# Kernel tuning notes

Hardware: AMD Instinct MI355X
Metric: run time of the kernel (lower is better)

Reference implementation:

```python
import jax, jax.numpy as jnp
import numpy as np

N = 768
C = 256  # in_features == out_features (required by Linear(in_features+3, 1))

def _leaky(x):
    return jnp.where(x >= 0, x, 0.2 * x)

def setup_inputs() -> dict:
    key = jax.random.key(0)
    ks = jax.random.split(key, 10)
    features = jax.random.normal(ks[0], (N, C), dtype=jnp.float32)
    coordinates = jax.random.normal(ks[1], (N, 3), dtype=jnp.float32)
    adj = jax.random.uniform(ks[2], (N, N), dtype=jnp.float32)  # unused by forward, kept for signature fidelity
    # Learned params
    FC = jax.random.normal(ks[3], (C, C), dtype=jnp.float32) * (1.414 / jnp.sqrt(C))
    # Conv1d(2,1,kernel=1): weight [out=1, in=2, k=1] -> 2 scalars + bias
    fc_w = jax.random.normal(ks[4], (2,), dtype=jnp.float32) * 0.5
    fc_b = jax.random.normal(ks[5], (1,), dtype=jnp.float32) * 0.1
    sc_w = jax.random.normal(ks[6], (2,), dtype=jnp.float32) * 0.5
    sc_b = jax.random.normal(ks[7], (1,), dtype=jnp.float32) * 0.1
    # Linear(C+3, 1)
    lin_w = jax.random.normal(ks[8], (C + 3,), dtype=jnp.float32) * (1.0 / jnp.sqrt(C + 3))
    lin_b = jax.random.normal(ks[9], (1,), dtype=jnp.float32) * 0.1
    return {"features": features, "coordinates": coordinates, "adj": adj,
            "FC": FC, "fc_w": fc_w, "fc_b": fc_b, "sc_w": sc_w, "sc_b": sc_b,
            "lin_w": lin_w, "lin_b": lin_b}

def reference(features, coordinates, adj, FC, fc_w, fc_b, sc_w, sc_b, lin_w, lin_b):
    n = features.shape[0]
    f_input = features @ FC  # [N, C]
    # torch's repeat(1,N).view + repeat(N,1) builds pairs (i, j); the 1x1 Conv1d over
    # the 2 stacked channels is exactly w0*x_i + w1*x_j + b, then LeakyReLU(0.2).
    f_map = _leaky(fc_w[0] * f_input[:, None, :] + fc_w[1] * f_input[None, :, :] + fc_b[0])  # [N,N,C]
    s_map = _leaky(sc_w[0] * coordinates[:, None, :] + sc_w[1] * coordinates[None, :, :] + sc_b[0])  # [N,N,3]
    # Linear(C+3, 1) on cat([f_map, s_map], -1), then LeakyReLU -> [N, N]
    scores = _leaky(jnp.einsum('ijc,c->ij', f_map, lin_w[:f_input.shape[1]])
                    + jnp.einsum('ijk,k->ij', s_map, lin_w[f_input.shape[1]:])
                    + lin_b[0])
    attention = jax.nn.softmax(scores, axis=1)  # row softmax (dim=1)
    h_prime = attention @ f_input  # [N, C]
    return jax.nn.elu(h_prime)  # concat=True path
```

## Files before the change

kernel.cpp:

```cpp
#include <hip/hip_runtime.h>
#include <math.h>

#define NN 768
#define CC 256
#define TI 3
#define RT 12
#define JCC 256
#define NJC 3
#define PSTR 20

__device__ __forceinline__ float leaky(float x) { return x >= 0.0f ? x : 0.2f * x; }

__device__ __forceinline__ float waveMax(float v) {
    #pragma unroll
    for (int o = 32; o > 0; o >>= 1) v = fmaxf(v, __shfl_xor(v, o, 64));
    return v;
}
__device__ __forceinline__ float waveSum(float v) {
    #pragma unroll
    for (int o = 32; o > 0; o >>= 1) v += __shfl_xor(v, o, 64);
    return v;
}

__device__ __forceinline__ void acc_row(float4& a, float ur, float w4, const float4& gv) {
    a.x = fmaf(w4, fabsf(ur + gv.x), a.x);
    a.y = fmaf(w4, fabsf(ur + gv.y), a.y);
    a.z = fmaf(w4, fabsf(ur + gv.z), a.z);
    a.w = fmaf(w4, fabsf(ur + gv.w), a.w);
}
__device__ __forceinline__ void fma4(float4& h, float e, const float4& fv) {
    h.x = fmaf(e, fv.x, h.x);
    h.y = fmaf(e, fv.y, h.y);
    h.z = fmaf(e, fv.z, h.z);
    h.w = fmaf(e, fv.w, h.w);
}

__global__ __launch_bounds__(768) void k_prep(
    const float* __restrict__ features,
    const float* __restrict__ FC,
    const float* __restrict__ fc_w,
    const float* __restrict__ fc_b,
    const float* __restrict__ lin_w,
    float* __restrict__ f,
    float* __restrict__ g,
    float* __restrict__ D0,
    float* __restrict__ D1,
    float4* __restrict__ ut4)
{
    __shared__ float sA[TI * CC];
    __shared__ float sF[TI * CC];
    __shared__ float sredD[12], sredW[12];

    const int t  = threadIdx.x;
    const int r  = t >> 8;
    const int c  = t & 255;
    const int i0 = blockIdx.x * TI;

    sA[r * CC + c] = features[(i0 + r) * CC + c];
    __syncthreads();

    float a = 0.f;
    const float* fcp = FC + c;
    const float* ap  = sA + r * CC;
    #pragma unroll 8
    for (int k = 0; k < CC; ++k)
        a = fmaf(ap[k], fcp[k * CC], a);

    const float w1 = fc_w[1], b = fc_b[0];
    f[(i0 + r) * CC + c] = a;
    g[c * NN + i0 + r]   = fmaf(w1, a, b);
    sF[r * CC + c] = a;

    const float lw = lin_w[c];
    float dv = waveSum(lw * a);
    float wv = waveSum(lw);
    const int wid = t >> 6;
    if ((t & 63) == 0) { sredD[wid] = dv; sredW[wid] = wv; }
    __syncthreads();
    if (t < TI) {
        float D = sredD[t*4] + sredD[t*4+1] + sredD[t*4+2] + sredD[t*4+3];
        float W = sredW[t*4] + sredW[t*4+1] + sredW[t*4+2] + sredW[t*4+3];
        D0[i0 + t] = fc_w[0] * D;
        D1[i0 + t] = fmaf(w1, D, b * W);
    }
    if (t < CC) {
        const float w0 = fc_w[0];
        ut4[blockIdx.x * CC + t] = make_float4(w0 * sF[t],
                                               w0 * sF[CC + t],
                                               w0 * sF[2*CC + t],
                                               0.4f * lin_w[t]);
    }
}

__global__ __launch_bounds__(256) void k_attn(
    const float* __restrict__ f,
    const float* __restrict__ g,
    const float4* __restrict__ ut4,
    const float* __restrict__ D0,
    const float* __restrict__ D1,
    const float* __restrict__ coords,
    const float* __restrict__ sc_w,
    const float* __restrict__ sc_b,
    const float* __restrict__ lin_w,
    const float* __restrict__ lin_b,
    float* __restrict__ hp,
    float* __restrict__ Mp,
    float* __restrict__ Lp)
{
    __shared__ float4 su4[4][CC];
    __shared__ float  sred[4][RT][CC];
    __shared__ float  pe[JCC][PSTR];
    __shared__ float  sredm[4][RT];
    __shared__ float  sreds[4][RT];

    const int t    = threadIdx.x;
    const int it   = blockIdx.x & 63;
    const int jc   = blockIdx.x >> 6;
    const int i0   = it * RT;
    const int jb   = jc * JCC;
    const int w    = t >> 6;
    const int lane = t & 63;

    #pragma unroll
    for (int q = 0; q < 4; ++q)
        su4[q][t] = ut4[(size_t)(it * 4 + q) * CC + t];
    __syncthreads();

    float4 acc[RT];
    #pragma unroll
    for (int r = 0; r < RT; ++r) acc[r] = make_float4(0.f, 0.f, 0.f, 0.f);
    const float4* gq = (const float4*)g + (size_t)(w << 6) * (NN/4) + (jb >> 2) + lane;
    #pragma unroll 4
    for (int cc = 0; cc < 64; ++cc) {
        float4 gv = gq[(size_t)cc * (NN/4)];
        const int c = (w << 6) + cc;
        #pragma unroll
        for (int q = 0; q < 4; ++q) {
            float4 u = su4[q][c];
            acc_row(acc[3*q+0], u.x, u.w, gv);
            acc_row(acc[3*q+1], u.y, u.w, gv);
            acc_row(acc[3*q+2], u.z, u.w, gv);
        }
    }
    #pragma unroll
    for (int r = 0; r < RT; ++r)
        *(float4*)&sred[w][r][4*lane] = acc[r];
    __syncthreads();

    const int j = jb + t;
    const float sw0 = sc_w[0], sw1 = sc_w[1], sb = sc_b[0], lb = lin_b[0];
    const float lw30 = lin_w[CC], lw31 = lin_w[CC+1], lw32 = lin_w[CC+2];
    const float cj0 = fmaf(sw1, coords[j*3+0], sb);
    const float cj1 = fmaf(sw1, coords[j*3+1], sb);
    const float cj2 = fmaf(sw1, coords[j*3+2], sb);
    const float d1  = D1[j];
    float scv[RT];
    #pragma unroll
    for (int r = 0; r < RT; ++r) {
        const int i = i0 + r;
        float a = sred[0][r][t] + sred[1][r][t] + sred[2][r][t] + sred[3][r][t];
        float sd = lw30 * leaky(fmaf(sw0, coords[i*3+0], cj0))
                 + lw31 * leaky(fmaf(sw0, coords[i*3+1], cj1))
                 + lw32 * leaky(fmaf(sw0, coords[i*3+2], cj2));
        scv[r] = leaky(a + sd + 0.6f * (D0[i] + d1) + lb);
    }

    #pragma unroll
    for (int r = 0; r < RT; ++r) {
        float v = waveMax(scv[r]);
        if (lane == 0) sredm[w][r] = v;
    }
    __syncthreads();
    float m[RT];
    #pragma unroll
    for (int r = 0; r < RT; ++r)
        m[r] = fmaxf(fmaxf(sredm[0][r], sredm[1][r]),
                     fmaxf(sredm[2][r], sredm[3][r]));
    float e[RT];
    #pragma unroll
    for (int r = 0; r < RT; ++r) {
        e[r] = __expf(scv[r] - m[r]);
        pe[t][r] = e[r];
    }
    #pragma unroll
    for (int r = 0; r < RT; ++r) {
        float v = waveSum(e[r]);
        if (lane == 0) sreds[w][r] = v;
    }
    __syncthreads();
    if (t < RT) {
        float l  = sreds[0][t] + sreds[1][t] + sreds[2][t] + sreds[3][t];
        float mm = fmaxf(fmaxf(sredm[0][t], sredm[1][t]),
                         fmaxf(sredm[2][t], sredm[3][t]));
        Mp[(i0 + t) * NJC + jc] = mm;
        Lp[(i0 + t) * NJC + jc] = l;
    }

    float4 h[RT];
    #pragma unroll
    for (int r = 0; r < RT; ++r) h[r] = make_float4(0.f, 0.f, 0.f, 0.f);
    const float4* f4 = (const float4*)f;
    const int jsl = w * 64;
    #pragma unroll 2
    for (int jx = 0; jx < 64; ++jx) {
        const int jl = jsl + jx;
        float4 fv = f4[(size_t)(jb + jl) * 64 + lane];
        const float4* pe4 = (const float4*)&pe[jl][0];
        float4 e0 = pe4[0], e1 = pe4[1], e2 = pe4[2];
        fma4(h[0],  e0.x, fv); fma4(h[1],  e0.y, fv);
        fma4(h[2],  e0.z, fv); fma4(h[3],  e0.w, fv);
        fma4(h[4],  e1.x, fv); fma4(h[5],  e1.y, fv);
        fma4(h[6],  e1.z, fv); fma4(h[7],  e1.w, fv);
        fma4(h[8],  e2.x, fv); fma4(h[9],  e2.y, fv);
        fma4(h[10], e2.z, fv); fma4(h[11], e2.w, fv);
    }
    #pragma unroll
    for (int r = 0; r < RT; ++r)
        *(float4*)&sred[w][r][4*lane] = h[r];
    __syncthreads();

    #pragma unroll
    for (int r = 0; r < RT; ++r) {
        float hh = sred[0][r][t] + sred[1][r][t] + sred[2][r][t] + sred[3][r][t];
        hp[((size_t)jc * NN + i0 + r) * CC + t] = hh;
    }
}

__global__ __launch_bounds__(256) void k_comb(
    const float* __restrict__ hp,
    const float* __restrict__ Mp,
    const float* __restrict__ Lp,
    float* __restrict__ out)
{
    const int t = threadIdx.x;
    const int i = blockIdx.x;

    float m0 = Mp[i*NJC+0], m1 = Mp[i*NJC+1], m2 = Mp[i*NJC+2];
    float M  = fmaxf(fmaxf(m0, m1), m2);
    float w0 = __expf(m0 - M), w1 = __expf(m1 - M), w2 = __expf(m2 - M);
    float den = w0*Lp[i*NJC+0] + w1*Lp[i*NJC+1] + w2*Lp[i*NJC+2];
    float inv = 1.0f / den;

    float num = w0 * hp[((size_t)0*NN + i)*CC + t]
              + w1 * hp[((size_t)1*NN + i)*CC + t]
              + w2 * hp[((size_t)2*NN + i)*CC + t];
    float v = num * inv;
    out[i*CC + t] = (v > 0.f) ? v : (__expf(v) - 1.0f);
}

extern "C" void kernel_launch(void* const* d_in, const int* in_sizes, int n_in,
                              void* d_out, int out_size, void* d_ws, size_t ws_size,
                              hipStream_t stream) {
    const float* features = (const float*)d_in[0];
    const float* coords   = (const float*)d_in[1];
    const float* FC       = (const float*)d_in[3];
    const float* fc_w     = (const float*)d_in[4];
    const float* fc_b     = (const float*)d_in[5];
    const float* sc_w     = (const float*)d_in[6];
    const float* sc_b     = (const float*)d_in[7];
    const float* lin_w    = (const float*)d_in[8];
    const float* lin_b    = (const float*)d_in[9];
    float* out = (float*)d_out;

    float* f  = (float*)d_ws;
    float* g  = f  + NN*CC;
    float* D0 = g  + CC*NN;
    float* D1 = D0 + NN;
    float* Mp = D1 + NN;
    float* Lp = Mp + NN*NJC;
    float* hp = Lp + NN*NJC;
    float4* ut4;
    {
        size_t off = (size_t)((char*)(hp + (size_t)NJC*NN*CC) - (char*)d_ws);
        off = (off + 15) & ~(size_t)15;
        ut4 = (float4*)((char*)d_ws + off);
    }

    k_prep<<<NN/TI, 768, 0, stream>>>(features, FC, fc_w, fc_b, lin_w, f, g, D0, D1, ut4);
    k_attn<<<(NN/RT)*NJC, 256, 0, stream>>>(f, g, ut4, D0, D1, coords, sc_w, sc_b,
                                            lin_w, lin_b, hp, Mp, Lp);
    k_comb<<<NN, 256, 0, stream>>>(hp, Mp, Lp, out);
}
```

Measured before the change: 128.8 us.

## Halve attention row and column tiles and broadcast u via readlane

```diff
diff --git a/kernel.cpp b/kernel.cpp
--- a/kernel.cpp
+++ b/kernel.cpp
@@ -4,12 +4,15 @@
 #define NN 768
 #define CC 256
 #define TI 3
-#define RT 12
-#define JCC 256
-#define NJC 3
-#define PSTR 20
+#define RT 6
+#define JC 128
+#define NJC 6
 
 __device__ __forceinline__ float leaky(float x) { return x >= 0.0f ? x : 0.2f * x; }
+
+__device__ __forceinline__ float rl(float v, int l) {
+    return __uint_as_float(__builtin_amdgcn_readlane(__float_as_uint(v), l));
+}
 
 __device__ __forceinline__ float waveMax(float v) {
     #pragma unroll
@@ -22,12 +25,6 @@
     return v;
 }
 
-__device__ __forceinline__ void acc_row(float4& a, float ur, float w4, const float4& gv) {
-    a.x = fmaf(w4, fabsf(ur + gv.x), a.x);
-    a.y = fmaf(w4, fabsf(ur + gv.y), a.y);
-    a.z = fmaf(w4, fabsf(ur + gv.z), a.z);
-    a.w = fmaf(w4, fabsf(ur + gv.w), a.w);
-}
 __device__ __forceinline__ void fma4(float4& h, float e, const float4& fv) {
     h.x = fmaf(e, fv.x, h.x);
     h.y = fmaf(e, fv.y, h.y);
@@ -107,121 +104,133 @@
     float* __restrict__ Mp,
     float* __restrict__ Lp)
 {
-    __shared__ float4 su4[4][CC];
-    __shared__ float  sred[4][RT][CC];
-    __shared__ float  pe[JCC][PSTR];
-    __shared__ float  sredm[4][RT];
-    __shared__ float  sreds[4][RT];
+    __shared__ float spart[4][RT][JC];
+    __shared__ float hpart[4][RT][CC];
+    __shared__ float pe[JC][8];
+    __shared__ float sredm[4][3];
+    __shared__ float sreds[4][3];
 
     const int t    = threadIdx.x;
-    const int it   = blockIdx.x & 63;
-    const int jc   = blockIdx.x >> 6;
+    const int it   = blockIdx.x & 127;
+    const int jc   = blockIdx.x >> 7;
     const int i0   = it * RT;
-    const int jb   = jc * JCC;
+    const int jb   = jc * JC;
     const int w    = t >> 6;
     const int lane = t & 63;
 
-    #pragma unroll
-    for (int q = 0; q < 4; ++q)
-        su4[q][t] = ut4[(size_t)(it * 4 + q) * CC + t];
-    __syncthreads();
-
-    float4 acc[RT];
-    #pragma unroll
-    for (int r = 0; r < RT; ++r) acc[r] = make_float4(0.f, 0.f, 0.f, 0.f);
-    const float4* gq = (const float4*)g + (size_t)(w << 6) * (NN/4) + (jb >> 2) + lane;
-    #pragma unroll 4
+    float4 ur0 = ut4[(size_t)(it*2 + 0) * CC + (w << 6) + lane];
+    float4 ur1 = ut4[(size_t)(it*2 + 1) * CC + (w << 6) + lane];
+
+    float2 acc[RT];
+    #pragma unroll
+    for (int r = 0; r < RT; ++r) acc[r] = make_float2(0.f, 0.f);
+    const float2* gq = (const float2*)g + (size_t)(w << 6) * (NN/2) + (jb >> 1) + lane;
+    #pragma unroll 8
     for (int cc = 0; cc < 64; ++cc) {
-        float4 gv = gq[(size_t)cc * (NN/4)];
-        const int c = (w << 6) + cc;
-        #pragma unroll
-        for (int q = 0; q < 4; ++q) {
-            float4 u = su4[q][c];
-            acc_row(acc[3*q+0], u.x, u.w, gv);
-            acc_row(acc[3*q+1], u.y, u.w, gv);
-            acc_row(acc[3*q+2], u.z, u.w, gv);
-        }
-    }
-    #pragma unroll
-    for (int r = 0; r < RT; ++r)
-        *(float4*)&sred[w][r][4*lane] = acc[r];
-    __syncthreads();
-
-    const int j = jb + t;
+        float2 gv = gq[cc * (NN/2)];
+        float w4 = rl(ur0.w, cc);
+        float u0 = rl(ur0.x, cc), u1 = rl(ur0.y, cc), u2 = rl(ur0.z, cc);
+        float u3 = rl(ur1.x, cc), u4 = rl(ur1.y, cc), u5 = rl(ur1.z, cc);
+        acc[0].x = fmaf(w4, fabsf(u0 + gv.x), acc[0].x);
+        acc[0].y = fmaf(w4, fabsf(u0 + gv.y), acc[0].y);
+        acc[1].x = fmaf(w4, fabsf(u1 + gv.x), acc[1].x);
+        acc[1].y = fmaf(w4, fabsf(u1 + gv.y), acc[1].y);
+        acc[2].x = fmaf(w4, fabsf(u2 + gv.x), acc[2].x);
+        acc[2].y = fmaf(w4, fabsf(u2 + gv.y), acc[2].y);
+        acc[3].x = fmaf(w4, fabsf(u3 + gv.x), acc[3].x);
+        acc[3].y = fmaf(w4, fabsf(u3 + gv.y), acc[3].y);
+        acc[4].x = fmaf(w4, fabsf(u4 + gv.x), acc[4].x);
+        acc[4].y = fmaf(w4, fabsf(u4 + gv.y), acc[4].y);
+        acc[5].x = fmaf(w4, fabsf(u5 + gv.x), acc[5].x);
+        acc[5].y = fmaf(w4, fabsf(u5 + gv.y), acc[5].y);
+    }
+    #pragma unroll
+    for (int r = 0; r < RT; ++r) {
+        spart[w][r][2*lane+0] = acc[r].x;
+        spart[w][r][2*lane+1] = acc[r].y;
+    }
+    __syncthreads();
+
+    const int jl   = t & 127;
+    const int half = t >> 7;
+    const int rb   = 3 * half;
+    const int j    = jb + jl;
+    float accs[3];
+    #pragma unroll
+    for (int rr = 0; rr < 3; ++rr)
+        accs[rr] = spart[0][rb+rr][jl] + spart[1][rb+rr][jl]
+                 + spart[2][rb+rr][jl] + spart[3][rb+rr][jl];
+
     const float sw0 = sc_w[0], sw1 = sc_w[1], sb = sc_b[0], lb = lin_b[0];
     const float lw30 = lin_w[CC], lw31 = lin_w[CC+1], lw32 = lin_w[CC+2];
     const float cj0 = fmaf(sw1, coords[j*3+0], sb);
     const float cj1 = fmaf(sw1, coords[j*3+1], sb);
     const float cj2 = fmaf(sw1, coords[j*3+2], sb);
     const float d1  = D1[j];
-    float scv[RT];
-    #pragma unroll
-    for (int r = 0; r < RT; ++r) {
-        const int i = i0 + r;
-        float a = sred[0][r][t] + sred[1][r][t] + sred[2][r][t] + sred[3][r][t];
+    float scv[3];
+    #pragma unroll
+    for (int rr = 0; rr < 3; ++rr) {
+        const int i = i0 + rb + rr;
         float sd = lw30 * leaky(fmaf(sw0, coords[i*3+0], cj0))
                  + lw31 * leaky(fmaf(sw0, coords[i*3+1], cj1))
                  + lw32 * leaky(fmaf(sw0, coords[i*3+2], cj2));
-        scv[r] = leaky(a + sd + 0.6f * (D0[i] + d1) + lb);
-    }
-
-    #pragma unroll
-    for (int r = 0; r < RT; ++r) {
-        float v = waveMax(scv[r]);
-        if (lane == 0) sredm[w][r] = v;
-    }
-    __syncthreads();
-    float m[RT];
-    #pragma unroll
-    for (int r = 0; r < RT; ++r)
-        m[r] = fmaxf(fmaxf(sredm[0][r], sredm[1][r]),
-                     fmaxf(sredm[2][r], sredm[3][r]));
-    float e[RT];
-    #pragma unroll
-    for (int r = 0; r < RT; ++r) {
-        e[r] = __expf(scv[r] - m[r]);
-        pe[t][r] = e[r];
-    }
-    #pragma unroll
-    for (int r = 0; r < RT; ++r) {
-        float v = waveSum(e[r]);
-        if (lane == 0) sreds[w][r] = v;
-    }
-    __syncthreads();
-    if (t < RT) {
-        float l  = sreds[0][t] + sreds[1][t] + sreds[2][t] + sreds[3][t];
-        float mm = fmaxf(fmaxf(sredm[0][t], sredm[1][t]),
-                         fmaxf(sredm[2][t], sredm[3][t]));
-        Mp[(i0 + t) * NJC + jc] = mm;
-        Lp[(i0 + t) * NJC + jc] = l;
+        scv[rr] = leaky(accs[rr] + sd + 0.6f * (D0[i] + d1) + lb);
+    }
+
+    #pragma unroll
+    for (int rr = 0; rr < 3; ++rr) {
+        float v = waveMax(scv[rr]);
+        if (lane == 0) sredm[w][rr] = v;
+    }
+    __syncthreads();
+    float m[3];
+    #pragma unroll
+    for (int rr = 0; rr < 3; ++rr)
+        m[rr] = fmaxf(sredm[2*half][rr], sredm[2*half+1][rr]);
+    float e[3];
+    #pragma unroll
+    for (int rr = 0; rr < 3; ++rr) {
+        e[rr] = __expf(scv[rr] - m[rr]);
+        pe[jl][rb + rr] = e[rr];
+    }
+    #pragma unroll
+    for (int rr = 0; rr < 3; ++rr) {
+        float v = waveSum(e[rr]);
+        if (lane == 0) sreds[w][rr] = v;
+    }
+    __syncthreads();
+    if (jl == 0) {
+        #pragma unroll
+        for (int rr = 0; rr < 3; ++rr) {
+            float l = sreds[2*half][rr] + sreds[2*half+1][rr];
+            Mp[(i0 + rb + rr) * NJC + jc] = m[rr];
+            Lp[(i0 + rb + rr) * NJC + jc] = l;
+        }
     }
 
     float4 h[RT];
     #pragma unroll
     for (int r = 0; r < RT; ++r) h[r] = make_float4(0.f, 0.f, 0.f, 0.f);
     const float4* f4 = (const float4*)f;
-    const int jsl = w * 64;
-    #pragma unroll 2
-    for (int jx = 0; jx < 64; ++jx) {
-        const int jl = jsl + jx;
-        float4 fv = f4[(size_t)(jb + jl) * 64 + lane];
-        const float4* pe4 = (const float4*)&pe[jl][0];
-        float4 e0 = pe4[0], e1 = pe4[1], e2 = pe4[2];
-        fma4(h[0],  e0.x, fv); fma4(h[1],  e0.y, fv);
-        fma4(h[2],  e0.z, fv); fma4(h[3],  e0.w, fv);
-        fma4(h[4],  e1.x, fv); fma4(h[5],  e1.y, fv);
-        fma4(h[6],  e1.z, fv); fma4(h[7],  e1.w, fv);
-        fma4(h[8],  e2.x, fv); fma4(h[9],  e2.y, fv);
-        fma4(h[10], e2.z, fv); fma4(h[11], e2.w, fv);
+    const int jsl = w << 5;
+    #pragma unroll 4
+    for (int jx = 0; jx < 32; ++jx) {
+        const int jl2 = jsl + jx;
+        float4 fv = f4[(size_t)(jb + jl2) * 64 + lane];
+        const float4* p4 = (const float4*)&pe[jl2][0];
+        float4 eA = p4[0];
+        float4 eB = p4[1];
+        fma4(h[0], eA.x, fv); fma4(h[1], eA.y, fv); fma4(h[2], eA.z, fv);
+        fma4(h[3], eA.w, fv); fma4(h[4], eB.x, fv); fma4(h[5], eB.y, fv);
     }
     #pragma unroll
     for (int r = 0; r < RT; ++r)
-        *(float4*)&sred[w][r][4*lane] = h[r];
+        *(float4*)&hpart[w][r][4*lane] = h[r];
     __syncthreads();
 
     #pragma unroll
     for (int r = 0; r < RT; ++r) {
-        float hh = sred[0][r][t] + sred[1][r][t] + sred[2][r][t] + sred[3][r][t];
+        float hh = hpart[0][r][t] + hpart[1][r][t] + hpart[2][r][t] + hpart[3][r][t];
         hp[((size_t)jc * NN + i0 + r) * CC + t] = hh;
     }
 }
@@ -235,15 +244,24 @@
     const int t = threadIdx.x;
     const int i = blockIdx.x;
 
-    float m0 = Mp[i*NJC+0], m1 = Mp[i*NJC+1], m2 = Mp[i*NJC+2];
-    float M  = fmaxf(fmaxf(m0, m1), m2);
-    float w0 = __expf(m0 - M), w1 = __expf(m1 - M), w2 = __expf(m2 - M);
-    float den = w0*Lp[i*NJC+0] + w1*Lp[i*NJC+1] + w2*Lp[i*NJC+2];
+    float mv[NJC];
+    #pragma unroll
+    for (int k = 0; k < NJC; ++k) mv[k] = Mp[i*NJC + k];
+    float M = mv[0];
+    #pragma unroll
+    for (int k = 1; k < NJC; ++k) M = fmaxf(M, mv[k]);
+    float wk[NJC], den = 0.f;
+    #pragma unroll
+    for (int k = 0; k < NJC; ++k) {
+        wk[k] = __expf(mv[k] - M);
+        den = fmaf(wk[k], Lp[i*NJC + k], den);
+    }
     float inv = 1.0f / den;
 
-    float num = w0 * hp[((size_t)0*NN + i)*CC + t]
-              + w1 * hp[((size_t)1*NN + i)*CC + t]
-              + w2 * hp[((size_t)2*NN + i)*CC + t];
+    float num = 0.f;
+    #pragma unroll
+    for (int k = 0; k < NJC; ++k)
+        num = fmaf(wk[k], hp[((size_t)k*NN + i)*CC + t], num);
     float v = num * inv;
     out[i*CC + t] = (v > 0.f) ? v : (__expf(v) - 1.0f);
 }
```

Measured after the change: 116.0 us. -10.0%, faster.
